# Performance work log

Measured on AMD Instinct MI355X. Metric: run time of the kernel, lower is better.

The kernel has to match this reference:

```python
import jax, jax.numpy as jnp
import numpy as np

GT_MASK_LEN = 128   # processor_dct.gt_mask_len
N_KEEP = 256        # processor_dct.n_keep


def _zigzag_flat_positions(n):
    """Row-major flat index of the k-th element in JPEG zigzag order of an n x n grid."""
    order = []
    for s in range(2 * n - 1):
        if s % 2 == 0:  # even diagonals traverse up-right
            for i in range(min(s, n - 1), max(-1, s - n), -1):
                order.append((i, s - i))
        else:
            for j in range(min(s, n - 1), max(-1, s - n), -1):
                order.append((s - j, j))
    return np.array([i * n + j for (i, j) in order], dtype=np.int64)


def _dct_matrix(n):
    """Orthonormal DCT-II matrix C (cv2.dct). cv2.idct(Y) == C.T @ Y @ C in 2-D."""
    k = np.arange(n)[:, None].astype(np.float64)
    m = np.arange(n)[None, :].astype(np.float64)
    C = np.sqrt(2.0 / n) * np.cos(np.pi * (2 * m + 1) * k / (2 * n))
    C[0, :] = np.sqrt(1.0 / n)
    return C.astype(np.float32)

_ZZ_POS = jnp.asarray(_zigzag_flat_positions(GT_MASK_LEN)[:N_KEEP])
_DCT_C = jnp.asarray(_dct_matrix(GT_MASK_LEN))


def setup_inputs() -> dict:
    key = jax.random.key(0)
    k1, k2, k3, k4 = jax.random.split(key, 4)
    B, R, C = 8, 300, 91
    pred_logits = jax.random.normal(k1, (B, R, C), dtype=jnp.float32)
    pred_boxes = jax.random.uniform(k2, (B, R, 4), dtype=jnp.float32) * 0.5 + 0.25
    pred_vectors = jax.random.normal(k3, (B, R, N_KEEP), dtype=jnp.float32)
    target_sizes = jax.random.randint(k4, (B, 2), 512, 1334, dtype=jnp.int32)
    return {"pred_logits": pred_logits, "pred_boxes": pred_boxes,
            "pred_vectors": pred_vectors, "target_sizes": target_sizes}


def reference(pred_logits, pred_boxes, pred_vectors, target_sizes):
    L = GT_MASK_LEN
    # --- classification scores ---
    prob = jax.nn.sigmoid(pred_logits)            # [B,R,C]
    scores = prob.max(axis=2)                     # [B,R]
    labels = prob.argmax(axis=2)                  # [B,R] int
    # --- boxes: cxcywh -> xyxy, rescale to image size ---
    cx, cy, w, h = jnp.split(pred_boxes, 4, axis=-1)
    boxes = jnp.concatenate([cx - 0.5 * w, cy - 0.5 * h,
                             cx + 0.5 * w, cy + 0.5 * h], axis=-1)  # [B,R,4]
    ts = target_sizes.astype(jnp.float32)
    img_h, img_w = ts[:, 0], ts[:, 1]
    scale_fct = jnp.stack([img_w, img_h, img_w, img_h], axis=1)     # [B,4]
    boxes = boxes * scale_fct[:, None, :]
    # --- masks: inverse zigzag scatter + batched separable 2-D IDCT ---
    B, R, _ = pred_vectors.shape
    flat = jnp.zeros((B, R, L * L), dtype=pred_vectors.dtype)
    flat = flat.at[:, :, _ZZ_POS].set(pred_vectors)
    coef = flat.reshape(B, R, L, L)
    # cv2.idct(Y) = C^T Y C (orthonormal DCT-III)
    re_mask = jnp.einsum('iu,bruv,vj->brij', _DCT_C.T, coef, _DCT_C)  # [B,R,L,L]
    max_v = re_mask.max(axis=(-2, -1), keepdims=True)
    min_v = re_mask.min(axis=(-2, -1), keepdims=True)
    masks = jnp.where(re_mask > (max_v + min_v) * 0.5, 1.0, 0.0).astype(jnp.float32)
    return scores, labels, boxes, masks
```

## Files before the change

kernel.cpp:

```cpp
#include <hip/hip_runtime.h>
#include <math.h>

#define NROWS 2400
#define NCLS  91
#define L     128
#define KSUB  23
#define NKEEP 256

#define TAB_OFF  2944
#define M1_OFF   2944
#define COEF_OFF 5888
#define RED_OFF  6440
#define SMEM_FLOATS 6456

__global__ void __launch_bounds__(512, 6)
postproc_kernel(const float* __restrict__ logits,
                const float* __restrict__ pboxes,
                const float* __restrict__ vecs,
                const int*   __restrict__ tsz,
                float* __restrict__ out)
{
    __shared__ float smem[SMEM_FLOATS];
    const int br  = blockIdx.x;
    const int tid = threadIdx.x;

    if (tid < 64) {
        const float* lrow = logits + (size_t)br * NCLS;
        float p = 1.0f / (1.0f + expf(-lrow[tid]));
        int   bi = tid;
        if (tid < NCLS - 64) {
            float p2 = 1.0f / (1.0f + expf(-lrow[tid + 64]));
            if (p2 > p) { p = p2; bi = tid + 64; }
        }
        #pragma unroll
        for (int off = 32; off > 0; off >>= 1) {
            float po = __shfl_xor(p, off, 64);
            int   io = __shfl_xor(bi, off, 64);
            if (po > p || (po == p && io < bi)) { p = po; bi = io; }
        }
        if (tid == 0) {
            out[br] = p;
            out[NROWS + br] = (float)bi;
            const int b = br / 300;
            const float W = (float)tsz[2 * b + 1];
            const float H = (float)tsz[2 * b + 0];
            const float4 bx = *(const float4*)(pboxes + (size_t)br * 4);
            float4 o;
            o.x = (bx.x - 0.5f * bx.z) * W;
            o.y = (bx.y - 0.5f * bx.w) * H;
            o.z = (bx.x + 0.5f * bx.z) * W;
            o.w = (bx.y + 0.5f * bx.w) * H;
            *(float4*)(out + 2 * NROWS + (size_t)br * 4) = o;
        }
    }

    double* tab = (double*)&smem[TAB_OFF];
    if (tid < 512) tab[tid] = cos((3.14159265358979323846 / 256.0) * (double)tid);
    __syncthreads();

    {
        const double s0 = sqrt(1.0 / 128.0);
        for (int idx = tid; idx < KSUB * L; idx += 512) {
            const int u = idx >> 7, m = idx & 127;
            float v;
            if (u == 0) v = (float)s0;
            else        v = (float)(0.125 * tab[((2 * m + 1) * u) & 511]);
            smem[idx] = v;
        }
    }
    float* coef = &smem[COEF_OFF];
    for (int t = tid; t < KSUB * 24; t += 512) {
        const int u = t / 24, v = t - u * 24;
        const int s = u + v;
        if (v == 23 || s > 22 || (s == 22 && u < 20)) coef[t] = 0.0f;
    }
    if (tid < NKEEP) {
        const int k = tid;
        int s = 0;
        while ((s + 1) * (s + 2) / 2 <= k) ++s;
        const int r = k - s * (s + 1) / 2;
        const int u  = (s & 1) ? r : (s - r);
        const int vv = (s & 1) ? (s - r) : r;
        coef[u * 24 + vv] = vecs[(size_t)br * NKEEP + k];
    }
    __syncthreads();

    float* M1 = &smem[M1_OFF];
    {
        const int i = tid & 127;
        const int g = tid >> 7;
        float cs[KSUB];
        #pragma unroll
        for (int u = 0; u < KSUB; ++u) cs[u] = smem[u * L + i];

        const int vbase = g * 6;
        float a[6];
        #pragma unroll
        for (int v = 0; v < 6; ++v) a[v] = 0.0f;
        if (g < 3) {
            #pragma unroll
            for (int u = 0; u < KSUB; ++u) {
                const float2 c0 = *(const float2*)&coef[u * 24 + vbase + 0];
                const float2 c1 = *(const float2*)&coef[u * 24 + vbase + 2];
                const float2 c2 = *(const float2*)&coef[u * 24 + vbase + 4];
                const float cu = cs[u];
                a[0] += cu * c0.x; a[1] += cu * c0.y;
                a[2] += cu * c1.x; a[3] += cu * c1.y;
                a[4] += cu * c2.x; a[5] += cu * c2.y;
            }
            #pragma unroll
            for (int v = 0; v < 6; ++v) M1[(vbase + v) * L + i] = a[v];
        } else {
            #pragma unroll
            for (int u = 0; u < KSUB; ++u) {
                const float2 c0 = *(const float2*)&coef[u * 24 + 18];
                const float2 c1 = *(const float2*)&coef[u * 24 + 20];
                const float  c2 = coef[u * 24 + 22];
                const float cu = cs[u];
                a[0] += cu * c0.x; a[1] += cu * c0.y;
                a[2] += cu * c1.x; a[3] += cu * c1.y;
                a[4] += cu * c2;
            }
            #pragma unroll
            for (int v = 0; v < 5; ++v) M1[(18 + v) * L + i] = a[v];
        }
    }
    __syncthreads();

    const int tx = tid & 31, iy = tid >> 5;
    const int j0 = tx << 2, i0 = iy << 3;
    float acc[8][4];
    #pragma unroll
    for (int r = 0; r < 8; ++r)
        #pragma unroll
        for (int q = 0; q < 4; ++q) acc[r][q] = 0.0f;

    for (int v = 0; v < KSUB; ++v) {
        const float4 c = *(const float4*)&smem[v * L + j0];
        #pragma unroll
        for (int g = 0; g < 2; ++g) {
            const float4 m = *(const float4*)&M1[v * L + i0 + 4 * g];
            acc[4*g+0][0] += m.x * c.x; acc[4*g+0][1] += m.x * c.y;
            acc[4*g+0][2] += m.x * c.z; acc[4*g+0][3] += m.x * c.w;
            acc[4*g+1][0] += m.y * c.x; acc[4*g+1][1] += m.y * c.y;
            acc[4*g+1][2] += m.y * c.z; acc[4*g+1][3] += m.y * c.w;
            acc[4*g+2][0] += m.z * c.x; acc[4*g+2][1] += m.z * c.y;
            acc[4*g+2][2] += m.z * c.z; acc[4*g+2][3] += m.z * c.w;
            acc[4*g+3][0] += m.w * c.x; acc[4*g+3][1] += m.w * c.y;
            acc[4*g+3][2] += m.w * c.z; acc[4*g+3][3] += m.w * c.w;
        }
    }

    float mn = acc[0][0], mx = acc[0][0];
    #pragma unroll
    for (int r = 0; r < 8; ++r)
        #pragma unroll
        for (int q = 0; q < 4; ++q) {
            mn = fminf(mn, acc[r][q]);
            mx = fmaxf(mx, acc[r][q]);
        }
    #pragma unroll
    for (int off = 32; off > 0; off >>= 1) {
        mn = fminf(mn, __shfl_xor(mn, off, 64));
        mx = fmaxf(mx, __shfl_xor(mx, off, 64));
    }
    const int w = tid >> 6;
    if ((tid & 63) == 0) { smem[RED_OFF + w] = mn; smem[RED_OFF + 8 + w] = mx; }
    __syncthreads();
    float gmn = smem[RED_OFF + 0], gmx = smem[RED_OFF + 8];
    #pragma unroll
    for (int k = 1; k < 8; ++k) {
        gmn = fminf(gmn, smem[RED_OFF + k]);
        gmx = fmaxf(gmx, smem[RED_OFF + 8 + k]);
    }
    const float thr = (gmx + gmn) * 0.5f;

    float* omask = out + 6 * NROWS + (size_t)br * (L * L);
    #pragma unroll
    for (int r = 0; r < 8; ++r) {
        float4 o;
        o.x = acc[r][0] > thr ? 1.0f : 0.0f;
        o.y = acc[r][1] > thr ? 1.0f : 0.0f;
        o.z = acc[r][2] > thr ? 1.0f : 0.0f;
        o.w = acc[r][3] > thr ? 1.0f : 0.0f;
        *(float4*)&omask[(i0 + r) * L + j0] = o;
    }
}

extern "C" void kernel_launch(void* const* d_in, const int* in_sizes, int n_in,
                              void* d_out, int out_size, void* d_ws, size_t ws_size,
                              hipStream_t stream)
{
    const float* logits = (const float*)d_in[0];
    const float* pboxes = (const float*)d_in[1];
    const float* vecs   = (const float*)d_in[2];
    const int*   tsz    = (const int*)d_in[3];
    float* out = (float*)d_out;
    (void)d_ws; (void)ws_size; (void)in_sizes; (void)n_in; (void)out_size;

    postproc_kernel<<<dim3(NROWS), dim3(512), 0, stream>>>(logits, pboxes, vecs, tsz, out);
}
```

Before: 187.1 us.

## Split IDCT into two kernels with first-pass results staged in global workspace

The single fused kernel is split in two. The first kernel computes the first IDCT pass and writes the 128x24 intermediate for each row to a global workspace, and block 0 also writes the cosine table there. The second kernel keeps the cosine columns in registers and reads the intermediate as float4 rows, so it needs no LDS for that data. The aim is to lower shared-memory pressure and raise occupancy, at the cost of an extra launch and about 29 MB of global write and read traffic. The second kernel also relies on block 0 of the first having written the table before it reads it.

```diff
diff --git a/kernel.cpp b/kernel.cpp
--- a/kernel.cpp
+++ b/kernel.cpp
@@ -7,20 +7,21 @@
 #define KSUB  23
 #define NKEEP 256
 
+#define WS_M1_OFF 4096
+
 #define TAB_OFF  2944
-#define M1_OFF   2944
-#define COEF_OFF 5888
-#define RED_OFF  6440
-#define SMEM_FLOATS 6456
-
-__global__ void __launch_bounds__(512, 6)
-postproc_kernel(const float* __restrict__ logits,
-                const float* __restrict__ pboxes,
-                const float* __restrict__ vecs,
-                const int*   __restrict__ tsz,
-                float* __restrict__ out)
+#define COEF_OFF 3968
+#define K1_SMEM  4520
+
+__global__ void __launch_bounds__(512)
+k1_stage1(const float* __restrict__ logits,
+          const float* __restrict__ pboxes,
+          const float* __restrict__ vecs,
+          const int*   __restrict__ tsz,
+          float* __restrict__ ws,
+          float* __restrict__ out)
 {
-    __shared__ float smem[SMEM_FLOATS];
+    __shared__ float smem[K1_SMEM];
     const int br  = blockIdx.x;
     const int tid = threadIdx.x;
 
@@ -85,7 +86,10 @@
     }
     __syncthreads();
 
-    float* M1 = &smem[M1_OFF];
+    if (br == 0) {
+        for (int t = tid; t < KSUB * L; t += 512) ws[t] = smem[t];
+    }
+
     {
         const int i = tid & 127;
         const int g = tid >> 7;
@@ -93,6 +97,7 @@
         #pragma unroll
         for (int u = 0; u < KSUB; ++u) cs[u] = smem[u * L + i];
 
+        float* dst = ws + WS_M1_OFF + ((size_t)br * 128 + i) * 24;
         const int vbase = g * 6;
         float a[6];
         #pragma unroll
@@ -108,8 +113,9 @@
                 a[2] += cu * c1.x; a[3] += cu * c1.y;
                 a[4] += cu * c2.x; a[5] += cu * c2.y;
             }
-            #pragma unroll
-            for (int v = 0; v < 6; ++v) M1[(vbase + v) * L + i] = a[v];
+            *(float2*)(dst + vbase + 0) = make_float2(a[0], a[1]);
+            *(float2*)(dst + vbase + 2) = make_float2(a[2], a[3]);
+            *(float2*)(dst + vbase + 4) = make_float2(a[4], a[5]);
         } else {
             #pragma unroll
             for (int u = 0; u < KSUB; ++u) {
@@ -121,69 +127,96 @@
                 a[2] += cu * c1.x; a[3] += cu * c1.y;
                 a[4] += cu * c2;
             }
-            #pragma unroll
-            for (int v = 0; v < 5; ++v) M1[(18 + v) * L + i] = a[v];
-        }
-    }
-    __syncthreads();
-
-    const int tx = tid & 31, iy = tid >> 5;
-    const int j0 = tx << 2, i0 = iy << 3;
-    float acc[8][4];
-    #pragma unroll
-    for (int r = 0; r < 8; ++r)
-        #pragma unroll
-        for (int q = 0; q < 4; ++q) acc[r][q] = 0.0f;
-
-    for (int v = 0; v < KSUB; ++v) {
-        const float4 c = *(const float4*)&smem[v * L + j0];
-        #pragma unroll
-        for (int g = 0; g < 2; ++g) {
-            const float4 m = *(const float4*)&M1[v * L + i0 + 4 * g];
-            acc[4*g+0][0] += m.x * c.x; acc[4*g+0][1] += m.x * c.y;
-            acc[4*g+0][2] += m.x * c.z; acc[4*g+0][3] += m.x * c.w;
-            acc[4*g+1][0] += m.y * c.x; acc[4*g+1][1] += m.y * c.y;
-            acc[4*g+1][2] += m.y * c.z; acc[4*g+1][3] += m.y * c.w;
-            acc[4*g+2][0] += m.z * c.x; acc[4*g+2][1] += m.z * c.y;
-            acc[4*g+2][2] += m.z * c.z; acc[4*g+2][3] += m.z * c.w;
-            acc[4*g+3][0] += m.w * c.x; acc[4*g+3][1] += m.w * c.y;
-            acc[4*g+3][2] += m.w * c.z; acc[4*g+3][3] += m.w * c.w;
-        }
+            *(float2*)(dst + 18) = make_float2(a[0], a[1]);
+            *(float2*)(dst + 20) = make_float2(a[2], a[3]);
+            dst[22] = a[4];
+            dst[23] = 0.0f;
+        }
+    }
+}
+
+__global__ void __launch_bounds__(512)
+k2_stage2(const float* __restrict__ ws,
+          float* __restrict__ out)
+{
+    __shared__ float red[16];
+    const int br   = blockIdx.x;
+    const int tid  = threadIdx.x;
+    const int lane = tid & 63;
+    const int i0   = __builtin_amdgcn_readfirstlane((tid >> 6) * 16);
+
+    float2 creg[KSUB];
+    {
+        const float* cbase = ws + 2 * lane;
+        #pragma unroll
+        for (int v = 0; v < KSUB; ++v)
+            creg[v] = *(const float2*)(cbase + v * L);
+    }
+
+    float acc[16][2];
+    const float* mrow = ws + WS_M1_OFF + ((size_t)br * 128 + i0) * 24;
+
+    #pragma unroll 2
+    for (int r = 0; r < 16; ++r) {
+        const float4* m4 = (const float4*)(mrow + r * 24);
+        const float4 ma = m4[0], mb = m4[1], mc = m4[2];
+        const float4 md = m4[3], me = m4[4], mf = m4[5];
+        float a0 = 0.0f, a1 = 0.0f;
+        a0 += ma.x * creg[0].x;  a1 += ma.x * creg[0].y;
+        a0 += ma.y * creg[1].x;  a1 += ma.y * creg[1].y;
+        a0 += ma.z * creg[2].x;  a1 += ma.z * creg[2].y;
+        a0 += ma.w * creg[3].x;  a1 += ma.w * creg[3].y;
+        a0 += mb.x * creg[4].x;  a1 += mb.x * creg[4].y;
+        a0 += mb.y * creg[5].x;  a1 += mb.y * creg[5].y;
+        a0 += mb.z * creg[6].x;  a1 += mb.z * creg[6].y;
+        a0 += mb.w * creg[7].x;  a1 += mb.w * creg[7].y;
+        a0 += mc.x * creg[8].x;  a1 += mc.x * creg[8].y;
+        a0 += mc.y * creg[9].x;  a1 += mc.y * creg[9].y;
+        a0 += mc.z * creg[10].x; a1 += mc.z * creg[10].y;
+        a0 += mc.w * creg[11].x; a1 += mc.w * creg[11].y;
+        a0 += md.x * creg[12].x; a1 += md.x * creg[12].y;
+        a0 += md.y * creg[13].x; a1 += md.y * creg[13].y;
+        a0 += md.z * creg[14].x; a1 += md.z * creg[14].y;
+        a0 += md.w * creg[15].x; a1 += md.w * creg[15].y;
+        a0 += me.x * creg[16].x; a1 += me.x * creg[16].y;
+        a0 += me.y * creg[17].x; a1 += me.y * creg[17].y;
+        a0 += me.z * creg[18].x; a1 += me.z * creg[18].y;
+        a0 += me.w * creg[19].x; a1 += me.w * creg[19].y;
+        a0 += mf.x * creg[20].x; a1 += mf.x * creg[20].y;
+        a0 += mf.y * creg[21].x; a1 += mf.y * creg[21].y;
+        a0 += mf.z * creg[22].x; a1 += mf.z * creg[22].y;
+        acc[r][0] = a0; acc[r][1] = a1;
     }
 
     float mn = acc[0][0], mx = acc[0][0];
     #pragma unroll
-    for (int r = 0; r < 8; ++r)
-        #pragma unroll
-        for (int q = 0; q < 4; ++q) {
-            mn = fminf(mn, acc[r][q]);
-            mx = fmaxf(mx, acc[r][q]);
-        }
+    for (int r = 0; r < 16; ++r) {
+        mn = fminf(mn, fminf(acc[r][0], acc[r][1]));
+        mx = fmaxf(mx, fmaxf(acc[r][0], acc[r][1]));
+    }
     #pragma unroll
     for (int off = 32; off > 0; off >>= 1) {
         mn = fminf(mn, __shfl_xor(mn, off, 64));
         mx = fmaxf(mx, __shfl_xor(mx, off, 64));
     }
     const int w = tid >> 6;
-    if ((tid & 63) == 0) { smem[RED_OFF + w] = mn; smem[RED_OFF + 8 + w] = mx; }
+    if (lane == 0) { red[w] = mn; red[8 + w] = mx; }
     __syncthreads();
-    float gmn = smem[RED_OFF + 0], gmx = smem[RED_OFF + 8];
+    float gmn = red[0], gmx = red[8];
     #pragma unroll
     for (int k = 1; k < 8; ++k) {
-        gmn = fminf(gmn, smem[RED_OFF + k]);
-        gmx = fmaxf(gmx, smem[RED_OFF + 8 + k]);
+        gmn = fminf(gmn, red[k]);
+        gmx = fmaxf(gmx, red[8 + k]);
     }
     const float thr = (gmx + gmn) * 0.5f;
 
-    float* omask = out + 6 * NROWS + (size_t)br * (L * L);
-    #pragma unroll
-    for (int r = 0; r < 8; ++r) {
-        float4 o;
+    float* omask = out + 6 * NROWS + (size_t)br * (L * L) + 2 * lane;
+    #pragma unroll
+    for (int r = 0; r < 16; ++r) {
+        float2 o;
         o.x = acc[r][0] > thr ? 1.0f : 0.0f;
         o.y = acc[r][1] > thr ? 1.0f : 0.0f;
-        o.z = acc[r][2] > thr ? 1.0f : 0.0f;
-        o.w = acc[r][3] > thr ? 1.0f : 0.0f;
-        *(float4*)&omask[(i0 + r) * L + j0] = o;
+        *(float2*)(omask + (size_t)(i0 + r) * L) = o;
     }
 }
 
@@ -196,7 +229,9 @@
     const float* vecs   = (const float*)d_in[2];
     const int*   tsz    = (const int*)d_in[3];
     float* out = (float*)d_out;
-    (void)d_ws; (void)ws_size; (void)in_sizes; (void)n_in; (void)out_size;
-
-    postproc_kernel<<<dim3(NROWS), dim3(512), 0, stream>>>(logits, pboxes, vecs, tsz, out);
+    float* ws  = (float*)d_ws;
+    (void)in_sizes; (void)n_in; (void)out_size; (void)ws_size;
+
+    k1_stage1<<<dim3(NROWS), dim3(512), 0, stream>>>(logits, pboxes, vecs, tsz, ws, out);
+    k2_stage2<<<dim3(NROWS), dim3(512), 0, stream>>>(ws, out);
 }
```

New measurement: 224.5 us. 20.0% more time.
